# Kernel optimization log

Measured on AMD Instinct MI355X. Metric: run time of the kernel, lower is better.

Reference implementation:

```python
import jax, jax.numpy as jnp
import numpy as np

B, S, D, H = 4, 2048, 512, 4
HD = D // H
EPS = 1e-5


def layer_norm(x, gamma, beta):
    mu = jnp.mean(x, axis=-1, keepdims=True)
    var = jnp.mean(jnp.square(x - mu), axis=-1, keepdims=True)
    return (x - mu) * jax.lax.rsqrt(var + EPS) * gamma + beta


def setup_inputs() -> dict:
    key = jax.random.key(0)
    ks = jax.random.split(key, 16)
    s_in = 1.0 / np.sqrt(D)
    s_ex = 1.0 / np.sqrt(2 * D)
    return {
        "input_states": jax.random.normal(ks[0], (B, S, D), jnp.float32),
        "positions": jax.random.normal(ks[1], (B, S, 3), jnp.float32),
        "W_expand": jax.random.uniform(ks[2], (D, 2 * D), jnp.float32, -s_in, s_in),
        "b_expand": jax.random.uniform(ks[3], (2 * D,), jnp.float32, -s_in, s_in),
        "W_squeeze": jax.random.uniform(ks[4], (2 * D, D), jnp.float32, -s_ex, s_ex),
        "b_squeeze": jax.random.uniform(ks[5], (D,), jnp.float32, -s_ex, s_ex),
        "gamma": jnp.ones((D,), jnp.float32),
        "beta": jnp.zeros((D,), jnp.float32),
        "Wq": jax.random.uniform(ks[6], (D, D), jnp.float32, -s_in, s_in),
        "bq": jax.random.uniform(ks[7], (D,), jnp.float32, -s_in, s_in),
        "Wk": jax.random.uniform(ks[8], (D, D), jnp.float32, -s_in, s_in),
        "bk": jax.random.uniform(ks[9], (D,), jnp.float32, -s_in, s_in),
        "Wv": jax.random.uniform(ks[10], (D, D), jnp.float32, -s_in, s_in),
        "bv": jax.random.uniform(ks[11], (D,), jnp.float32, -s_in, s_in),
        "alpha": jnp.float32(0.1),
    }


def reference(input_states, positions, W_expand, b_expand, W_squeeze, b_squeeze,
              gamma, beta, Wq, bq, Wk, bk, Wv, bv, alpha):
    # FFN (expand -> relu -> squeeze) + residual + LayerNorm
    h = jax.nn.relu(input_states @ W_expand + b_expand)
    squeezed = h @ W_squeeze + b_squeeze
    se = layer_norm(input_states + squeezed, gamma, beta)

    # q/k/v projections, split heads: [B,H,S,HD]
    q = (se @ Wq + bq).reshape(B, S, H, HD).transpose(0, 2, 1, 3)
    k = (se @ Wk + bk).reshape(B, S, H, HD).transpose(0, 2, 1, 3)
    v = (se @ Wv + bv).reshape(B, S, H, HD).transpose(0, 2, 1, 3)

    scores = jnp.einsum('bhid,bhjd->bhij', q, k) / np.sqrt(HD)

    # squared pairwise distance bias: ||pi||^2 + ||pj||^2 - 2 pi.pj, broadcast over heads
    sq = jnp.sum(positions * positions, axis=-1)  # [B,S]
    dist2 = sq[:, :, None] + sq[:, None, :] - 2.0 * jnp.einsum('bic,bjc->bij', positions, positions)
    dist2 = jnp.maximum(dist2, 0.0)
    scores = scores - alpha * dist2[:, None, :, :]

    w = jax.nn.softmax(scores, axis=-1)
    ctx = jnp.einsum('bhij,bhjd->bhid', w, v)
    ctx = ctx.transpose(0, 2, 1, 3).reshape(B, S, D)

    # same LayerNorm params reused (self.norm applied twice in original)
    return layer_norm(se + ctx, gamma, beta)
```

## Files before the change

kernel.cpp:

```cpp
#include <hip/hip_runtime.h>

typedef __bf16 bf16_t;
typedef __attribute__((ext_vector_type(8))) __bf16 bf16x8;
typedef __attribute__((ext_vector_type(4))) __bf16 bf16x4;
typedef __attribute__((ext_vector_type(4))) float f32x4;
typedef __attribute__((ext_vector_type(16))) float f32x16;

constexpr int Bc = 4, Sc = 2048, Dc = 512, Hc = 4, HDc = 128;
constexpr int Mrows = Bc * Sc;

__device__ inline void gl2lds(const void* g, void* l) {
  __builtin_amdgcn_global_load_lds(
      (__attribute__((address_space(1))) void*)g,
      (__attribute__((address_space(3))) void*)l, 16, 0, 0);
}

__global__ __launch_bounds__(256) void prep_k(
    const float* __restrict__ X, bf16_t* __restrict__ xb,
    const float* __restrict__ pos, const float* __restrict__ alphap,
    bf16_t* __restrict__ Qbg, bf16_t* __restrict__ Kbg,
    const float* __restrict__ We, bf16_t* __restrict__ wtE,
    const float* __restrict__ Ws, bf16_t* __restrict__ wtS,
    const float* __restrict__ Wq, const float* __restrict__ Wk,
    const float* __restrict__ Wv, bf16_t* __restrict__ wtQKV) {
  const int bid = blockIdx.x;
  if (bid < 2048) {
    const long i = ((long)bid * 256 + threadIdx.x) * 8;
    const float4 a = *(const float4*)(X + i);
    const float4 c = *(const float4*)(X + i + 4);
    bf16x8 o;
    o[0] = (bf16_t)a.x; o[1] = (bf16_t)a.y; o[2] = (bf16_t)a.z; o[3] = (bf16_t)a.w;
    o[4] = (bf16_t)c.x; o[5] = (bf16_t)c.y; o[6] = (bf16_t)c.z; o[7] = (bf16_t)c.w;
    *(bf16x8*)(xb + i) = o;
    return;
  }
  if (bid < 2080) {
    const float ap = alphap[0] * 11.313708498984761f;
    const int i = (bid - 2048) * 256 + threadIdx.x;
    const int b = i >> 11, s = i & 2047;
    const float x = pos[(long)i * 3], y = pos[(long)i * 3 + 1], z = pos[(long)i * 3 + 2];
    const float m2 = -ap * (x * x + y * y + z * z);
    bf16x8 qlo = {}, klo = {}, zer = {};
    qlo[0] = (bf16_t)(2.f * ap * x); qlo[1] = (bf16_t)(2.f * ap * y);
    qlo[2] = (bf16_t)(2.f * ap * z); qlo[3] = (bf16_t)1.0f;
    klo[0] = (bf16_t)x; klo[1] = (bf16_t)y; klo[2] = (bf16_t)z; klo[3] = (bf16_t)m2;
    *(bf16x8*)(Qbg + (long)i * 16) = qlo;
    *(bf16x8*)(Qbg + (long)i * 16 + 8) = zer;
    const int t = s >> 6, kh = (s >> 5) & 1, key = s & 31;
    const long kb = ((long)(b * 32 + t) * 2 + kh) * 512 + key * 8;
    *(bf16x8*)(Kbg + kb) = klo;
    *(bf16x8*)(Kbg + kb + 256) = zer;
    return;
  }
  __shared__ float tile[32][33];
  const float* src; bf16_t* dst; int K, N, local;
  if (bid < 2592)      { src = We; dst = wtE; K = 512;  N = 1024; local = bid - 2080; }
  else if (bid < 3104) { src = Ws; dst = wtS; K = 1024; N = 512;  local = bid - 2592; }
  else if (bid < 3360) { src = Wq; dst = wtQKV;          K = 512; N = 512; local = bid - 3104; }
  else if (bid < 3616) { src = Wk; dst = wtQKV + 262144; K = 512; N = 512; local = bid - 3360; }
  else                 { src = Wv; dst = wtQKV + 524288; K = 512; N = 512; local = bid - 3616; }
  const int nb = N / 32;
  const int n0 = (local % nb) * 32, k0 = (local / nb) * 32;
  const int tx = threadIdx.x & 31, ty = threadIdx.x >> 5;
#pragma unroll
  for (int i = 0; i < 4; i++)
    tile[ty + i * 8][tx] = src[(long)(k0 + ty + i * 8) * N + n0 + tx];
  __syncthreads();
#pragma unroll
  for (int i = 0; i < 4; i++)
    dst[(long)(n0 + ty + i * 8) * K + k0 + tx] = (bf16_t)tile[tx][ty + i * 8];
}

template <int OMODE, int TN, int NB>
__global__ __launch_bounds__(256, (TN == 128) ? 2 : 3) void gemm128_k(
    const bf16_t* __restrict__ A, const bf16_t* __restrict__ Bt,
    const float* __restrict__ bias0, const float* __restrict__ bias1,
    const float* __restrict__ bias2, void* __restrict__ out0,
    void* __restrict__ out1, void* __restrict__ out2, int N, int K) {
  __shared__ bf16_t As[2][128 * 64];
  __shared__ bf16_t Bs[2][TN * 64];
  constexpr int MT = (TN == 128) ? 4 : 2;
  constexpr int BI = (TN == 128) ? 4 : 2;
  constexpr int MW = (TN == 128) ? 64 : 32;
  const int t = threadIdx.x;
  const int p = blockIdx.x;
  const int slot = p >> 3;
  const int by = (p & 7) + 8 * (slot / NB);
  const int bx = slot % NB;
  const int n0 = bx * TN, m0 = by * 128;
  const int lane = t & 63, wave = t >> 6;
  const int quad = lane >> 4, ln = lane & 15;
  const int wm = (TN == 128) ? (wave >> 1) : wave;
  const int wn = (TN == 128) ? (wave & 1) : 0;
  const int l8 = lane >> 3, g = lane & 7;
  const bf16_t* aseg = A + (long)(m0 + wave * 32 + l8) * K + (g ^ l8) * 8;
  const bf16_t* bseg = Bt + (long)(n0 + wave * (BI * 8) + l8) * K + (g ^ l8) * 8;
  auto stage = [&](int buf, int k0) {
#pragma unroll
    for (int i = 0; i < 4; i++)
      gl2lds(aseg + (long)i * 8 * K + k0, &As[buf][(wave * 32 + i * 8) * 64]);
#pragma unroll
    for (int i = 0; i < BI; i++)
      gl2lds(bseg + (long)i * 8 * K + k0, &Bs[buf][(wave * BI * 8 + i * 8) * 64]);
  };
  f32x4 acc[MT][4] = {};
  stage(0, 0);
  const int niter = K / 64;
  for (int it = 0; it < niter; it++) {
    const int cur = it & 1;
    __syncthreads();
    if (it + 1 < niter) stage(1 - cur, (it + 1) * 64);
#pragma unroll
    for (int kc = 0; kc < 2; kc++) {
      bf16x8 af[MT], bfr[4];
#pragma unroll
      for (int mt = 0; mt < MT; mt++)
        af[mt] = *(const bf16x8*)&As[cur][(wm * MW + mt * 16 + ln) * 64 +
                                          (((kc * 4 + quad) ^ (ln & 7)) * 8)];
#pragma unroll
      for (int nt = 0; nt < 4; nt++)
        bfr[nt] = *(const bf16x8*)&Bs[cur][(wn * 64 + nt * 16 + ln) * 64 +
                                           (((kc * 4 + quad) ^ (ln & 7)) * 8)];
#pragma unroll
      for (int mt = 0; mt < MT; mt++)
#pragma unroll
        for (int nt = 0; nt < 4; nt++)
          acc[mt][nt] = __builtin_amdgcn_mfma_f32_16x16x32_bf16(af[mt], bfr[nt],
                                                                acc[mt][nt], 0, 0, 0);
    }
  }
#pragma unroll
  for (int nt = 0; nt < 4; nt++) {
    const int gcol = n0 + wn * 64 + nt * 16 + ln;
    if constexpr (OMODE == 0 || OMODE == 1) {
      const float bv = bias0[gcol];
      bf16_t* o = (bf16_t*)out0;
#pragma unroll
      for (int mt = 0; mt < MT; mt++)
#pragma unroll
        for (int r = 0; r < 4; r++) {
          const int grow = m0 + wm * MW + mt * 16 + quad * 4 + r;
          float vv = acc[mt][nt][r] + bv;
          if constexpr (OMODE == 0) vv = vv > 0.f ? vv : 0.f;
          o[(long)grow * N + gcol] = (bf16_t)vv;
        }
    } else {
      const int which = gcol >> 9, n = gcol & 511;
      const int hh = n >> 7, hd = n & 127;
      const float bv = (which == 0 ? bias0 : which == 1 ? bias1 : bias2)[n];
      bf16_t* o = (bf16_t*)(which == 0 ? out0 : which == 1 ? out1 : out2);
#pragma unroll
      for (int mt = 0; mt < MT; mt++)
#pragma unroll
        for (int r = 0; r < 4; r++) {
          const int grow = m0 + wm * MW + mt * 16 + quad * 4 + r;
          const int b = grow >> 11, s = grow & 2047;
          const float vv = acc[mt][nt][r] + bv;
          long idx;
          if (which == 0) {
            idx = ((long)((b * Hc + hh) * Sc + s)) * HDc + hd;
          } else if (which == 1) {
            const int tt = s >> 6, kh = (s >> 5) & 1, key = s & 31;
            const int c = hd >> 4, lk = key + 32 * ((hd >> 3) & 1), j = hd & 7;
            idx = ((((long)((b * Hc + hh) * 32 + tt) * 2 + kh) * 8 + c) * 64 + lk) * 8 + j;
          } else {
            const int tt = s >> 6, ht2 = hd >> 5, kc2 = (s & 63) >> 4;
            const int kl = s & 15;
            const int klp = (kl & 3) | ((kl & 4) << 1) | ((kl & 8) >> 1);
            const int lk = (hd & 31) + 32 * (klp >> 3), j = klp & 7;
            idx = ((((long)((b * Hc + hh) * 32 + tt) * 4 + ht2) * 4 + kc2) * 64 + lk) * 8 + j;
          }
          o[idx] = (bf16_t)vv;
        }
    }
  }
}

template <int AF32, int OF32>
__global__ __launch_bounds__(256) void ln_k(const void* __restrict__ xa,
                                            const bf16_t* __restrict__ xb,
                                            const float* __restrict__ gamma,
                                            const float* __restrict__ beta,
                                            void* __restrict__ out) {
  const int wave = threadIdx.x >> 6, lane = threadIdx.x & 63;
  const long row = (long)blockIdx.x * 4 + wave;
  const int col0 = lane * 8;
  float vv[8];
  float s = 0.f, s2 = 0.f;
  const bf16x8 vb = *(const bf16x8*)(xb + row * Dc + col0);
  if constexpr (AF32) {
    const float* a = (const float*)xa + row * Dc + col0;
    const float4 a0 = *(const float4*)a;
    const float4 a1 = *(const float4*)(a + 4);
    const float xs[8] = {a0.x, a0.y, a0.z, a0.w, a1.x, a1.y, a1.z, a1.w};
#pragma unroll
    for (int j = 0; j < 8; j++) vv[j] = xs[j] + (float)vb[j];
  } else {
    const bf16x8 va = *(const bf16x8*)((const bf16_t*)xa + row * Dc + col0);
#pragma unroll
    for (int j = 0; j < 8; j++) vv[j] = (float)va[j] + (float)vb[j];
  }
#pragma unroll
  for (int j = 0; j < 8; j++) { s += vv[j]; s2 += vv[j] * vv[j]; }
#pragma unroll
  for (int off = 1; off < 64; off <<= 1) {
    s += __shfl_xor(s, off, 64);
    s2 += __shfl_xor(s2, off, 64);
  }
  const float mu = s * (1.f / Dc);
  const float var = s2 * (1.f / Dc) - mu * mu;
  const float rstd = rsqrtf(var + 1e-5f);
  const float4 g0 = *(const float4*)(gamma + col0);
  const float4 g1 = *(const float4*)(gamma + col0 + 4);
  const float4 b0 = *(const float4*)(beta + col0);
  const float4 b1 = *(const float4*)(beta + col0 + 4);
  const float gs[8] = {g0.x, g0.y, g0.z, g0.w, g1.x, g1.y, g1.z, g1.w};
  const float bs[8] = {b0.x, b0.y, b0.z, b0.w, b1.x, b1.y, b1.z, b1.w};
  if constexpr (OF32) {
    float* o = (float*)out + row * Dc + col0;
    float4 o0, o1;
    o0.x = (vv[0] - mu) * rstd * gs[0] + bs[0];
    o0.y = (vv[1] - mu) * rstd * gs[1] + bs[1];
    o0.z = (vv[2] - mu) * rstd * gs[2] + bs[2];
    o0.w = (vv[3] - mu) * rstd * gs[3] + bs[3];
    o1.x = (vv[4] - mu) * rstd * gs[4] + bs[4];
    o1.y = (vv[5] - mu) * rstd * gs[5] + bs[5];
    o1.z = (vv[6] - mu) * rstd * gs[6] + bs[6];
    o1.w = (vv[7] - mu) * rstd * gs[7] + bs[7];
    *(float4*)o = o0; *(float4*)(o + 4) = o1;
  } else {
    bf16x8 ob;
#pragma unroll
    for (int j = 0; j < 8; j++) ob[j] = (bf16_t)((vv[j] - mu) * rstd * gs[j] + bs[j]);
    *(bf16x8*)((bf16_t*)out + row * Dc + col0) = ob;
  }
}

__global__ __launch_bounds__(256, 2) void attn_k(const bf16_t* __restrict__ q,
                                                 const bf16_t* __restrict__ Kg,
                                                 const bf16_t* __restrict__ Vg,
                                                 const bf16_t* __restrict__ Qbg,
                                                 const bf16_t* __restrict__ Kbg,
                                                 bf16_t* __restrict__ ctx) {
  __shared__ bf16_t Ks[2][8192];
  __shared__ bf16_t Vts[2][8192];
  __shared__ bf16_t Kb[2][1024];
  __shared__ float RsD[4][32];
  const int t = threadIdx.x;
  const int p = blockIdx.x;
  const int qt = (p >> 3) & 31;
  const int gg = (p & 7) + 8 * (p >> 8);
  const int h = gg & 3, b = gg >> 2;
  const int q0 = qt * 64;
  const int wave = t >> 6, lane = t & 63;
  const int l31 = lane & 31, hb = lane >> 5;
  const int rh = wave & 1, kh = wave >> 1;
  const float scale_l2 = 1.4426950408889634f * 0.08838834764831845f;

  bf16x8 qf[8], qbf;
  const long qrow = (long)((b * Hc + h) * Sc + q0 + rh * 32 + l31);
#pragma unroll
  for (int c = 0; c < 8; c++)
    qf[c] = *(const bf16x8*)(q + qrow * HDc + c * 16 + hb * 8);
  qbf = *(const bf16x8*)(Qbg + (long)(b * Sc + q0 + rh * 32 + l31) * 16 + hb * 8);

  const bf16_t* ktile = Kg + (long)((b * Hc + h) * 32) * 8192 + lane * 8;
  const bf16_t* vtile = Vg + (long)((b * Hc + h) * 32) * 8192 + lane * 8;
  const bf16_t* kbtile = Kbg + (long)(b * 32) * 1024 + lane * 8;
  auto stage = [&](int buf) {
#pragma unroll
    for (int i = 0; i < 4; i++)
      gl2lds(ktile + (wave * 4 + i) * 512, &Ks[buf][(wave * 4 + i) * 512]);
#pragma unroll
    for (int i = 0; i < 4; i++)
      gl2lds(vtile + (wave * 4 + i) * 512, &Vts[buf][(wave * 4 + i) * 512]);
    if (wave < 2) gl2lds(kbtile + wave * 512, &Kb[buf][wave * 512]);
  };
  stage(0);
  ktile += 8192; vtile += 8192; kbtile += 1024;

  float rsl = 0.f;
  f32x16 accT[4] = {};

  for (int kt = 0; kt < Sc / 64; kt++) {
    const int cur = kt & 1;
    __syncthreads();
    if (kt < Sc / 64 - 1) {
      stage(1 - cur);
      ktile += 8192; vtile += 8192; kbtile += 1024;
    }
    f32x16 sa = {}, sb = {};
    __builtin_amdgcn_s_setprio(1);
#pragma unroll
    for (int c = 0; c < 4; c++) {
      const bf16x8 kf = *(const bf16x8*)&Ks[cur][(kh * 8 + c) * 512 + lane * 8];
      sa = __builtin_amdgcn_mfma_f32_32x32x16_bf16(kf, qf[c], sa, 0, 0, 0);
    }
#pragma unroll
    for (int c = 4; c < 8; c++) {
      const bf16x8 kf = *(const bf16x8*)&Ks[cur][(kh * 8 + c) * 512 + lane * 8];
      sb = __builtin_amdgcn_mfma_f32_32x32x16_bf16(kf, qf[c], sb, 0, 0, 0);
    }
    {
      const bf16x8 kbf = *(const bf16x8*)&Kb[cur][kh * 512 + lane * 8];
      sb = __builtin_amdgcn_mfma_f32_32x32x16_bf16(kbf, qbf, sb, 0, 0, 0);
    }
    __builtin_amdgcn_s_setprio(0);
    const f32x16 sacc = sa + sb;

    float pe[16];
#pragma unroll
    for (int i = 0; i < 16; i++) {
      pe[i] = __builtin_amdgcn_exp2f(sacc[i] * scale_l2);
      rsl += pe[i];
    }
    bf16x8 pf0, pf1;
#pragma unroll
    for (int j = 0; j < 8; j++) {
      pf0[j] = (bf16_t)pe[j];
      pf1[j] = (bf16_t)pe[8 + j];
    }

    __builtin_amdgcn_s_setprio(1);
#pragma unroll
    for (int ht = 0; ht < 4; ht++) {
      const bf16x8 v0 = *(const bf16x8*)&Vts[cur][(ht * 4 + kh * 2 + 0) * 512 + lane * 8];
      accT[ht] = __builtin_amdgcn_mfma_f32_32x32x16_bf16(v0, pf0, accT[ht], 0, 0, 0);
      const bf16x8 v1 = *(const bf16x8*)&Vts[cur][(ht * 4 + kh * 2 + 1) * 512 + lane * 8];
      accT[ht] = __builtin_amdgcn_mfma_f32_32x32x16_bf16(v1, pf1, accT[ht], 0, 0, 0);
    }
    __builtin_amdgcn_s_setprio(0);
  }
  __syncthreads();

  rsl += __shfl_xor(rsl, 32, 64);
  if (hb == 0) RsD[wave][l31] = rsl;
  float* Oc = (float*)&Ks[0][0];
  if (kh == 1) {
#pragma unroll
    for (int ht = 0; ht < 4; ht++)
#pragma unroll
      for (int r = 0; r < 16; r++) {
        const int hdp = (r & 3) + 8 * (r >> 2) + 4 * hb;
        Oc[(ht * 32 + hdp) * 64 + rh * 32 + l31] = accT[ht][r];
      }
  }
  __syncthreads();
  if (kh == 0) {
    const float rinv = 1.f / (RsD[wave][l31] + RsD[wave + 2][l31]);
    const long orow = (long)(b * Sc + q0 + rh * 32 + l31);
#pragma unroll
    for (int ht = 0; ht < 4; ht++)
#pragma unroll
      for (int g2 = 0; g2 < 4; g2++) {
        bf16x4 ov;
#pragma unroll
        for (int r0 = 0; r0 < 4; r0++) {
          const int hdp = r0 + 8 * g2 + 4 * hb;
          ov[r0] = (bf16_t)((accT[ht][g2 * 4 + r0] +
                             Oc[(ht * 32 + hdp) * 64 + rh * 32 + l31]) * rinv);
        }
        *(bf16x4*)(ctx + orow * Dc + h * HDc + ht * 32 + 8 * g2 + 4 * hb) = ov;
      }
  }
}

constexpr size_t SQB_OFF = 0;
constexpr size_t SEB_OFF = 8388608;
constexpr size_t Q_OFF = 16777216;
constexpr size_t K_OFF = 25165824;
constexpr size_t V_OFF = 33554432;
constexpr size_t XB_OFF = Q_OFF;
constexpr size_t H_OFF = K_OFF;
constexpr size_t QBG_OFF = 41943040;
constexpr size_t KBG_OFF = QBG_OFF + 262144;
constexpr size_t WTE_OFF = KBG_OFF + 262144;
constexpr size_t WTS_OFF = WTE_OFF + 1048576;
constexpr size_t WTQKV_OFF = WTS_OFF + 1048576;

extern "C" void kernel_launch(void* const* d_in, const int* in_sizes, int n_in,
                              void* d_out, int out_size, void* d_ws, size_t ws_size,
                              hipStream_t stream) {
  const float* X = (const float*)d_in[0];
  const float* pos = (const float*)d_in[1];
  const float* W_expand = (const float*)d_in[2];
  const float* b_expand = (const float*)d_in[3];
  const float* W_squeeze = (const float*)d_in[4];
  const float* b_squeeze = (const float*)d_in[5];
  const float* gamma = (const float*)d_in[6];
  const float* beta = (const float*)d_in[7];
  const float* Wq = (const float*)d_in[8];
  const float* bq = (const float*)d_in[9];
  const float* Wk = (const float*)d_in[10];
  const float* bk = (const float*)d_in[11];
  const float* Wv = (const float*)d_in[12];
  const float* bv = (const float*)d_in[13];
  const float* alphap = (const float*)d_in[14];

  char* ws = (char*)d_ws;
  bf16_t* sqb = (bf16_t*)(ws + SQB_OFF);
  bf16_t* ctxb = (bf16_t*)(ws + SQB_OFF);
  bf16_t* seb = (bf16_t*)(ws + SEB_OFF);
  bf16_t* qbg = (bf16_t*)(ws + QBG_OFF);
  bf16_t* kbg = (bf16_t*)(ws + KBG_OFF);
  bf16_t* qb = (bf16_t*)(ws + Q_OFF);
  bf16_t* kb = (bf16_t*)(ws + K_OFF);
  bf16_t* vb = (bf16_t*)(ws + V_OFF);
  bf16_t* xbb = (bf16_t*)(ws + XB_OFF);
  bf16_t* hb = (bf16_t*)(ws + H_OFF);
  bf16_t* wtE = (bf16_t*)(ws + WTE_OFF);
  bf16_t* wtS = (bf16_t*)(ws + WTS_OFF);
  bf16_t* wtQKV = (bf16_t*)(ws + WTQKV_OFF);

  prep_k<<<3872, 256, 0, stream>>>(X, xbb, pos, alphap, qbg, kbg,
                                   W_expand, wtE, W_squeeze, wtS, Wq, Wk, Wv, wtQKV);
  gemm128_k<0, 128, 8><<<512, 256, 0, stream>>>(
      xbb, wtE, b_expand, nullptr, nullptr, hb, nullptr, nullptr, 1024, 512);
  gemm128_k<1, 64, 8><<<512, 256, 0, stream>>>(
      hb, wtS, b_squeeze, nullptr, nullptr, sqb, nullptr, nullptr, 512, 1024);
  ln_k<1, 0><<<Mrows / 4, 256, 0, stream>>>(X, sqb, gamma, beta, seb);
  gemm128_k<2, 128, 12><<<768, 256, 0, stream>>>(
      seb, wtQKV, bq, bk, bv, qb, kb, vb, 1536, 512);
  attn_k<<<512, 256, 0, stream>>>(qb, kb, vb, qbg, kbg, ctxb);
  ln_k<0, 1><<<Mrows / 4, 256, 0, stream>>>(seb, ctxb, gamma, beta, (float*)d_out);

  (void)in_sizes; (void)n_in; (void)out_size; (void)ws_size;
}
```

Before: 214.5 us.

## Load V and distance-bias tiles directly into registers instead of LDS

V tiles and the positional K-bias fragments are now loaded from global memory straight into per-wave registers, double-buffered in explicit A/B register sets, rather than staged through shared memory. Only K still goes through LDS. The loop is unrolled by two to alternate buffers without dynamic indexing. The intent is to cut LDS traffic and LDS footprint (possibly raising occupancy) and shorten the staging step. The cost is higher register pressure and global-load latency that now sits in the register path. Both kh-wave pairs fetch the same V data separately.

```diff
diff --git a/kernel.cpp b/kernel.cpp
--- a/kernel.cpp
+++ b/kernel.cpp
@@ -243,8 +243,6 @@
                                                  const bf16_t* __restrict__ Kbg,
                                                  bf16_t* __restrict__ ctx) {
   __shared__ bf16_t Ks[2][8192];
-  __shared__ bf16_t Vts[2][8192];
-  __shared__ bf16_t Kb[2][1024];
   __shared__ float RsD[4][32];
   const int t = threadIdx.x;
   const int p = blockIdx.x;
@@ -265,49 +263,50 @@
   qbf = *(const bf16x8*)(Qbg + (long)(b * Sc + q0 + rh * 32 + l31) * 16 + hb * 8);
 
   const bf16_t* ktile = Kg + (long)((b * Hc + h) * 32) * 8192 + lane * 8;
-  const bf16_t* vtile = Vg + (long)((b * Hc + h) * 32) * 8192 + lane * 8;
-  const bf16_t* kbtile = Kbg + (long)(b * 32) * 1024 + lane * 8;
-  auto stage = [&](int buf) {
+  const bf16_t* vbase = Vg + (long)((b * Hc + h) * 32) * 8192 + kh * 1024 + lane * 8;
+  const bf16_t* kbbase = Kbg + (long)(b * 32) * 1024 + kh * 512 + lane * 8;
+
+  auto stageK = [&](int buf) {
 #pragma unroll
     for (int i = 0; i < 4; i++)
       gl2lds(ktile + (wave * 4 + i) * 512, &Ks[buf][(wave * 4 + i) * 512]);
-#pragma unroll
-    for (int i = 0; i < 4; i++)
-      gl2lds(vtile + (wave * 4 + i) * 512, &Vts[buf][(wave * 4 + i) * 512]);
-    if (wave < 2) gl2lds(kbtile + wave * 512, &Kb[buf][wave * 512]);
   };
-  stage(0);
-  ktile += 8192; vtile += 8192; kbtile += 1024;
+  stageK(0);
+  ktile += 8192;
+
+  bf16x8 vA0, vA1, vA2, vA3, vA4, vA5, vA6, vA7, kbfA;
+  {
+    const bf16_t* vt = vbase;
+    vA0 = *(const bf16x8*)(vt);        vA1 = *(const bf16x8*)(vt + 512);
+    vA2 = *(const bf16x8*)(vt + 2048); vA3 = *(const bf16x8*)(vt + 2560);
+    vA4 = *(const bf16x8*)(vt + 4096); vA5 = *(const bf16x8*)(vt + 4608);
+    vA6 = *(const bf16x8*)(vt + 6144); vA7 = *(const bf16x8*)(vt + 6656);
+    kbfA = *(const bf16x8*)(kbbase);
+  }
+  bf16x8 vB0, vB1, vB2, vB3, vB4, vB5, vB6, vB7, kbfB;
 
   float rsl = 0.f;
   f32x16 accT[4] = {};
 
-  for (int kt = 0; kt < Sc / 64; kt++) {
-    const int cur = kt & 1;
-    __syncthreads();
-    if (kt < Sc / 64 - 1) {
-      stage(1 - cur);
-      ktile += 8192; vtile += 8192; kbtile += 1024;
-    }
+  auto body = [&](const bf16_t* KsCur, const bf16x8& kbf, const bf16x8& w0,
+                  const bf16x8& w1, const bf16x8& w2, const bf16x8& w3,
+                  const bf16x8& w4, const bf16x8& w5, const bf16x8& w6,
+                  const bf16x8& w7) {
     f32x16 sa = {}, sb = {};
     __builtin_amdgcn_s_setprio(1);
 #pragma unroll
     for (int c = 0; c < 4; c++) {
-      const bf16x8 kf = *(const bf16x8*)&Ks[cur][(kh * 8 + c) * 512 + lane * 8];
+      const bf16x8 kf = *(const bf16x8*)&KsCur[(kh * 8 + c) * 512 + lane * 8];
       sa = __builtin_amdgcn_mfma_f32_32x32x16_bf16(kf, qf[c], sa, 0, 0, 0);
     }
 #pragma unroll
     for (int c = 4; c < 8; c++) {
-      const bf16x8 kf = *(const bf16x8*)&Ks[cur][(kh * 8 + c) * 512 + lane * 8];
+      const bf16x8 kf = *(const bf16x8*)&KsCur[(kh * 8 + c) * 512 + lane * 8];
       sb = __builtin_amdgcn_mfma_f32_32x32x16_bf16(kf, qf[c], sb, 0, 0, 0);
     }
-    {
-      const bf16x8 kbf = *(const bf16x8*)&Kb[cur][kh * 512 + lane * 8];
-      sb = __builtin_amdgcn_mfma_f32_32x32x16_bf16(kbf, qbf, sb, 0, 0, 0);
-    }
+    sb = __builtin_amdgcn_mfma_f32_32x32x16_bf16(kbf, qbf, sb, 0, 0, 0);
     __builtin_amdgcn_s_setprio(0);
     const f32x16 sacc = sa + sb;
-
     float pe[16];
 #pragma unroll
     for (int i = 0; i < 16; i++) {
@@ -316,20 +315,44 @@
     }
     bf16x8 pf0, pf1;
 #pragma unroll
-    for (int j = 0; j < 8; j++) {
-      pf0[j] = (bf16_t)pe[j];
-      pf1[j] = (bf16_t)pe[8 + j];
-    }
-
+    for (int j = 0; j < 8; j++) { pf0[j] = (bf16_t)pe[j]; pf1[j] = (bf16_t)pe[8 + j]; }
     __builtin_amdgcn_s_setprio(1);
-#pragma unroll
-    for (int ht = 0; ht < 4; ht++) {
-      const bf16x8 v0 = *(const bf16x8*)&Vts[cur][(ht * 4 + kh * 2 + 0) * 512 + lane * 8];
-      accT[ht] = __builtin_amdgcn_mfma_f32_32x32x16_bf16(v0, pf0, accT[ht], 0, 0, 0);
-      const bf16x8 v1 = *(const bf16x8*)&Vts[cur][(ht * 4 + kh * 2 + 1) * 512 + lane * 8];
-      accT[ht] = __builtin_amdgcn_mfma_f32_32x32x16_bf16(v1, pf1, accT[ht], 0, 0, 0);
-    }
+    accT[0] = __builtin_amdgcn_mfma_f32_32x32x16_bf16(w0, pf0, accT[0], 0, 0, 0);
+    accT[0] = __builtin_amdgcn_mfma_f32_32x32x16_bf16(w1, pf1, accT[0], 0, 0, 0);
+    accT[1] = __builtin_amdgcn_mfma_f32_32x32x16_bf16(w2, pf0, accT[1], 0, 0, 0);
+    accT[1] = __builtin_amdgcn_mfma_f32_32x32x16_bf16(w3, pf1, accT[1], 0, 0, 0);
+    accT[2] = __builtin_amdgcn_mfma_f32_32x32x16_bf16(w4, pf0, accT[2], 0, 0, 0);
+    accT[2] = __builtin_amdgcn_mfma_f32_32x32x16_bf16(w5, pf1, accT[2], 0, 0, 0);
+    accT[3] = __builtin_amdgcn_mfma_f32_32x32x16_bf16(w6, pf0, accT[3], 0, 0, 0);
+    accT[3] = __builtin_amdgcn_mfma_f32_32x32x16_bf16(w7, pf1, accT[3], 0, 0, 0);
     __builtin_amdgcn_s_setprio(0);
+  };
+
+  for (int kt2 = 0; kt2 < 16; kt2++) {
+    __syncthreads();
+    stageK(1);
+    ktile += 8192;
+    {
+      const bf16_t* vt = vbase + (long)(2 * kt2 + 1) * 8192;
+      vB0 = *(const bf16x8*)(vt);        vB1 = *(const bf16x8*)(vt + 512);
+      vB2 = *(const bf16x8*)(vt + 2048); vB3 = *(const bf16x8*)(vt + 2560);
+      vB4 = *(const bf16x8*)(vt + 4096); vB5 = *(const bf16x8*)(vt + 4608);
+      vB6 = *(const bf16x8*)(vt + 6144); vB7 = *(const bf16x8*)(vt + 6656);
+      kbfB = *(const bf16x8*)(kbbase + (long)(2 * kt2 + 1) * 1024);
+    }
+    body(&Ks[0][0], kbfA, vA0, vA1, vA2, vA3, vA4, vA5, vA6, vA7);
+    __syncthreads();
+    if (kt2 < 15) {
+      stageK(0);
+      ktile += 8192;
+      const bf16_t* vt = vbase + (long)(2 * kt2 + 2) * 8192;
+      vA0 = *(const bf16x8*)(vt);        vA1 = *(const bf16x8*)(vt + 512);
+      vA2 = *(const bf16x8*)(vt + 2048); vA3 = *(const bf16x8*)(vt + 2560);
+      vA4 = *(const bf16x8*)(vt + 4096); vA5 = *(const bf16x8*)(vt + 4608);
+      vA6 = *(const bf16x8*)(vt + 6144); vA7 = *(const bf16x8*)(vt + 6656);
+      kbfA = *(const bf16x8*)(kbbase + (long)(2 * kt2 + 2) * 1024);
+    }
+    body(&Ks[1][0], kbfB, vB0, vB1, vB2, vB3, vB4, vB5, vB6, vB7);
   }
   __syncthreads();
 
```

After: 217.6 us. No clear change (+1.5%).

## Load attention K/V fragments directly into registers with one-tile prefetch instead of LDS staging

Applied to the files above, without the earlier changes.

The attention kernel stops staging K, V and the positional key block through double-buffered shared memory. Each wave now reads its own MFMA fragments straight from global memory into registers, prefetching the next key tile after each MFMA group, which removes the per-iteration __syncthreads and the LDS round-trip. In exchange, waves that share a key half load the same data twice, and each iteration now waits on global-memory latency with only one tile of lookahead. It also adds register pressure. The final iteration prefetches one tile past the current head, which reads outside the buffer for the last head.

```diff
diff --git a/kernel.cpp b/kernel.cpp
--- a/kernel.cpp
+++ b/kernel.cpp
@@ -242,9 +242,7 @@
                                                  const bf16_t* __restrict__ Qbg,
                                                  const bf16_t* __restrict__ Kbg,
                                                  bf16_t* __restrict__ ctx) {
-  __shared__ bf16_t Ks[2][8192];
-  __shared__ bf16_t Vts[2][8192];
-  __shared__ bf16_t Kb[2][1024];
+  __shared__ float Oc[8192];
   __shared__ float RsD[4][32];
   const int t = threadIdx.x;
   const int p = blockIdx.x;
@@ -264,50 +262,41 @@
     qf[c] = *(const bf16x8*)(q + qrow * HDc + c * 16 + hb * 8);
   qbf = *(const bf16x8*)(Qbg + (long)(b * Sc + q0 + rh * 32 + l31) * 16 + hb * 8);
 
-  const bf16_t* ktile = Kg + (long)((b * Hc + h) * 32) * 8192 + lane * 8;
-  const bf16_t* vtile = Vg + (long)((b * Hc + h) * 32) * 8192 + lane * 8;
-  const bf16_t* kbtile = Kbg + (long)(b * 32) * 1024 + lane * 8;
-  auto stage = [&](int buf) {
-#pragma unroll
-    for (int i = 0; i < 4; i++)
-      gl2lds(ktile + (wave * 4 + i) * 512, &Ks[buf][(wave * 4 + i) * 512]);
-#pragma unroll
-    for (int i = 0; i < 4; i++)
-      gl2lds(vtile + (wave * 4 + i) * 512, &Vts[buf][(wave * 4 + i) * 512]);
-    if (wave < 2) gl2lds(kbtile + wave * 512, &Kb[buf][wave * 512]);
-  };
-  stage(0);
-  ktile += 8192; vtile += 8192; kbtile += 1024;
+  const bf16_t* kfb = Kg + (long)((b * Hc + h) * 32) * 8192 + (kh * 8) * 512 + lane * 8;
+  const bf16_t* vfb = Vg + (long)((b * Hc + h) * 32) * 8192 + kh * 1024 + lane * 8;
+  const bf16_t* kbb = Kbg + (long)(b * 32) * 1024 + kh * 512 + lane * 8;
+
+  bf16x8 kr[8], vr[8], kbr;
+#pragma unroll
+  for (int c = 0; c < 8; c++) kr[c] = *(const bf16x8*)(kfb + c * 512);
+  kbr = *(const bf16x8*)(kbb);
+#pragma unroll
+  for (int i = 0; i < 8; i++)
+    vr[i] = *(const bf16x8*)(vfb + (i >> 1) * 2048 + (i & 1) * 512);
 
   float rsl = 0.f;
   f32x16 accT[4] = {};
 
-  for (int kt = 0; kt < Sc / 64; kt++) {
-    const int cur = kt & 1;
-    __syncthreads();
-    if (kt < Sc / 64 - 1) {
-      stage(1 - cur);
-      ktile += 8192; vtile += 8192; kbtile += 1024;
-    }
+  for (int kt = 0; kt < 32; kt++) {
     f32x16 sa = {}, sb = {};
     __builtin_amdgcn_s_setprio(1);
 #pragma unroll
-    for (int c = 0; c < 4; c++) {
-      const bf16x8 kf = *(const bf16x8*)&Ks[cur][(kh * 8 + c) * 512 + lane * 8];
-      sa = __builtin_amdgcn_mfma_f32_32x32x16_bf16(kf, qf[c], sa, 0, 0, 0);
-    }
-#pragma unroll
-    for (int c = 4; c < 8; c++) {
-      const bf16x8 kf = *(const bf16x8*)&Ks[cur][(kh * 8 + c) * 512 + lane * 8];
-      sb = __builtin_amdgcn_mfma_f32_32x32x16_bf16(kf, qf[c], sb, 0, 0, 0);
-    }
+    for (int c = 0; c < 4; c++)
+      sa = __builtin_amdgcn_mfma_f32_32x32x16_bf16(kr[c], qf[c], sa, 0, 0, 0);
+#pragma unroll
+    for (int c = 4; c < 8; c++)
+      sb = __builtin_amdgcn_mfma_f32_32x32x16_bf16(kr[c], qf[c], sb, 0, 0, 0);
+    sb = __builtin_amdgcn_mfma_f32_32x32x16_bf16(kbr, qbf, sb, 0, 0, 0);
+    __builtin_amdgcn_s_setprio(0);
+    __builtin_amdgcn_sched_barrier(0);
     {
-      const bf16x8 kbf = *(const bf16x8*)&Kb[cur][kh * 512 + lane * 8];
-      sb = __builtin_amdgcn_mfma_f32_32x32x16_bf16(kbf, qbf, sb, 0, 0, 0);
-    }
-    __builtin_amdgcn_s_setprio(0);
+      const long noff = (long)(kt + 1) * 8192;
+#pragma unroll
+      for (int c = 0; c < 8; c++)
+        kr[c] = *(const bf16x8*)(kfb + noff + c * 512);
+      kbr = *(const bf16x8*)(kbb + (long)(kt + 1) * 1024);
+    }
     const f32x16 sacc = sa + sb;
-
     float pe[16];
 #pragma unroll
     for (int i = 0; i < 16; i++) {
@@ -316,26 +305,26 @@
     }
     bf16x8 pf0, pf1;
 #pragma unroll
-    for (int j = 0; j < 8; j++) {
-      pf0[j] = (bf16_t)pe[j];
-      pf1[j] = (bf16_t)pe[8 + j];
-    }
-
+    for (int j = 0; j < 8; j++) { pf0[j] = (bf16_t)pe[j]; pf1[j] = (bf16_t)pe[8 + j]; }
     __builtin_amdgcn_s_setprio(1);
 #pragma unroll
     for (int ht = 0; ht < 4; ht++) {
-      const bf16x8 v0 = *(const bf16x8*)&Vts[cur][(ht * 4 + kh * 2 + 0) * 512 + lane * 8];
-      accT[ht] = __builtin_amdgcn_mfma_f32_32x32x16_bf16(v0, pf0, accT[ht], 0, 0, 0);
-      const bf16x8 v1 = *(const bf16x8*)&Vts[cur][(ht * 4 + kh * 2 + 1) * 512 + lane * 8];
-      accT[ht] = __builtin_amdgcn_mfma_f32_32x32x16_bf16(v1, pf1, accT[ht], 0, 0, 0);
+      accT[ht] = __builtin_amdgcn_mfma_f32_32x32x16_bf16(vr[2 * ht], pf0, accT[ht], 0, 0, 0);
+      accT[ht] = __builtin_amdgcn_mfma_f32_32x32x16_bf16(vr[2 * ht + 1], pf1, accT[ht], 0, 0, 0);
     }
     __builtin_amdgcn_s_setprio(0);
+    __builtin_amdgcn_sched_barrier(0);
+    {
+      const long noff = (long)(kt + 1) * 8192;
+#pragma unroll
+      for (int i = 0; i < 8; i++)
+        vr[i] = *(const bf16x8*)(vfb + noff + (i >> 1) * 2048 + (i & 1) * 512);
+    }
   }
   __syncthreads();
 
   rsl += __shfl_xor(rsl, 32, 64);
   if (hb == 0) RsD[wave][l31] = rsl;
-  float* Oc = (float*)&Ks[0][0];
   if (kh == 1) {
 #pragma unroll
     for (int ht = 0; ht < 4; ht++)
```

Result: no change. 215.7 us (+0.6%).
